# Kernel optimization log

Hardware: AMD Instinct MI355X
Metric: run time of the kernel (lower is better)

The kernel has to match this reference:

```python
import jax, jax.numpy as jnp
import numpy as np

BLOCK = 128


def setup_inputs() -> dict:
    key = jax.random.key(0)
    k_x, k_w, k_s, k_b = jax.random.split(key, 4)
    B, S, IN, OUT = 2, 2048, 4096, 4096
    x = jax.random.normal(k_x, (B, S, IN), dtype=jnp.float32)
    # fp8-quantized weight values (simulate e4m3 rounding, keep fp32 storage)
    w = jax.random.normal(k_w, (OUT, IN), dtype=jnp.float32) * 0.02
    weight = w.astype(jnp.float8_e4m3fn).astype(jnp.float32)
    # per-128x128-block inverse scales
    weight_scale_inv = jax.random.uniform(
        k_s, (OUT // BLOCK, IN // BLOCK), dtype=jnp.float32, minval=0.5, maxval=1.5)
    bias = jax.random.normal(k_b, (OUT,), dtype=jnp.float32) * 0.01
    return {"x": x, "weight": weight, "weight_scale_inv": weight_scale_inv, "bias": bias}


def _dequant(weight, scale_inv):
    # weight: [O, I], scale_inv: [O/128, I/128] -> broadcast each scale over a 128x128 block
    O, I = weight.shape
    w = weight.reshape(O // BLOCK, BLOCK, I // BLOCK, BLOCK)
    w = w * scale_inv[:, None, :, None]
    return w.reshape(O, I)


def reference(x, weight, weight_scale_inv, bias):
    w_deq = _dequant(weight, weight_scale_inv)          # [O, I]
    out = jnp.einsum('bsi,oi->bso', x, w_deq)           # [B, S, O]
    return out + bias
```

## Files before the change

### kernel.cpp

```cpp
#include <hip/hip_runtime.h>
#include <hip/hip_bf16.h>
#include <stdint.h>

typedef __attribute__((ext_vector_type(4))) float f32x4;
typedef __attribute__((ext_vector_type(8))) short short8;

__device__ __forceinline__ ushort f2b(float f) {
    union { __hip_bfloat16 h; ushort u; } c;
    c.h = __float2bfloat16(f);
    return c.u;
}

__device__ __forceinline__ void gload_lds16(const void* g, void* lds) {
    __builtin_amdgcn_global_load_lds((const __attribute__((address_space(1))) void*)g,
                                     (__attribute__((address_space(3))) void*)lds,
                                     16, 0, 0);
}

#define BARRIER()  asm volatile("s_barrier" ::: "memory")
#define VMCNT0()   asm volatile("s_waitcnt vmcnt(0)" ::: "memory")

__global__ void conv_both_kernel(const float* __restrict__ x, ushort* __restrict__ xb, long n8x,
                                 const float* __restrict__ w, const float* __restrict__ sinv,
                                 ushort* __restrict__ wb, int K, int nbk, long n8w) {
    long i = (long)blockIdx.x * blockDim.x + threadIdx.x;
    if (blockIdx.y == 0) {
        if (i >= n8x) return;
        const float4* xv = (const float4*)x;
        float4 v0 = xv[i * 2], v1 = xv[i * 2 + 1];
        short8 r;
        r[0] = (short)f2b(v0.x); r[1] = (short)f2b(v0.y); r[2] = (short)f2b(v0.z); r[3] = (short)f2b(v0.w);
        r[4] = (short)f2b(v1.x); r[5] = (short)f2b(v1.y); r[6] = (short)f2b(v1.z); r[7] = (short)f2b(v1.w);
        *(short8*)&xb[i * 8] = r;
    } else {
        if (i >= n8w) return;
        long e = i * 8;
        int o, c;
        if (K == 4096) { o = (int)(e >> 12); c = (int)(e & 4095); }
        else { o = (int)(e / K); c = (int)(e - (long)o * K); }
        const float s = sinv[(o >> 7) * nbk + (c >> 7)];
        const float4* wv = (const float4*)(w + e);
        float4 v0 = wv[0], v1 = wv[1];
        short8 r;
        r[0] = (short)f2b(v0.x * s); r[1] = (short)f2b(v0.y * s); r[2] = (short)f2b(v0.z * s); r[3] = (short)f2b(v0.w * s);
        r[4] = (short)f2b(v1.x * s); r[5] = (short)f2b(v1.y * s); r[6] = (short)f2b(v1.z * s); r[7] = (short)f2b(v1.w * s);
        *(short8*)&wb[e] = r;
    }
}

__global__ __launch_bounds__(512, 2)
void gemm256_kernel(const ushort* __restrict__ A, const ushort* __restrict__ Bm,
                    const float* __restrict__ bias, float* __restrict__ C,
                    int M, int N, int K) {
    __shared__ alignas(16) short sm[2][32768];

    const int tid  = threadIdx.x;
    const int lane = tid & 63;
    const int wid  = tid >> 6;
    const int wr   = wid >> 2;
    const int wc   = wid & 3;
    const int nbn  = N >> 8;

    const int nwg = gridDim.x;
    const int swz = (blockIdx.x & 7) * (nwg >> 3) + (blockIdx.x >> 3);
    const int bm  = swz / nbn;
    const int bn  = swz % nbn;

    const short* gA = (const short*)A + (size_t)bm * 256 * K;
    const short* gB = (const short*)Bm + (size_t)bn * 256 * K;

    const int srow = wid * 8 + (lane >> 3);
    const int scol = ((lane & 7) ^ (lane >> 3)) << 3;

    auto STAGE_A = [&](int U, int kt, int buf) {
        const short* src = gA + (size_t)(U * 64 + srow) * K + kt * 64 + scol;
        gload_lds16(src, &sm[buf][U * 4096 + wid * 512]);
    };
    auto STAGE_B = [&](int U, int kt, int buf) {
        const short* src = gB + (size_t)(U * 64 + srow) * K + kt * 64 + scol;
        gload_lds16(src, &sm[buf][16384 + U * 4096 + wid * 512]);
    };

    auto LD_A = [&](const short* Ab, int mh, int kk, short8 (&a)[4]) {
#pragma unroll
        for (int m = 0; m < 4; ++m) {
            int row = wr * 128 + mh * 64 + m * 16 + (lane & 15);
            a[m] = *(const short8*)&Ab[row * 64 + ((kk * 32 + (lane >> 4) * 8) ^ ((lane & 7) << 3))];
        }
    };
    auto LD_B = [&](const short* Bb, int kk, short8 (&b)[4]) {
#pragma unroll
        for (int n = 0; n < 4; ++n) {
            int row = wc * 64 + n * 16 + (lane & 15);
            b[n] = *(const short8*)&Bb[row * 64 + ((kk * 32 + (lane >> 4) * 8) ^ ((lane & 7) << 3))];
        }
    };

    f32x4 acc[8][4] = {};

    auto MFMA_H = [&](int off, short8 (&af)[4], short8 (&bf)[4], int m0, int m1) {
#pragma unroll
        for (int m = m0; m < m1; ++m)
#pragma unroll
            for (int n = 0; n < 4; ++n)
                acc[off + m][n] = __builtin_amdgcn_mfma_f32_16x16x32_bf16(af[m], bf[n], acc[off + m][n], 0, 0, 0);
    };

    const int nkt = K >> 6;

    short8 aCur[4], bCur[4];

    auto KSTEP = [&](int t) {
        const int b  = t & 1;
        const int tb = b ^ 1;
        const short* Ab  = &sm[b][0];
        const short* Bb  = &sm[b][16384];
        const short* AbN = &sm[tb][0];
        const short* BbN = &sm[tb][16384];
        const int tn = (t + 1 < nkt) ? t + 1 : nkt - 1;

        short8 aB[4], aC[4], aD[4], bB[4];

        BARRIER();
        __builtin_amdgcn_s_setprio(1);
        MFMA_H(0, aCur, bCur, 0, 2);
        LD_A(Ab, 1, 0, aB);
        MFMA_H(0, aCur, bCur, 2, 4);
        __builtin_amdgcn_s_setprio(0);
        STAGE_B(0, tn, tb); STAGE_B(1, tn, tb);
        STAGE_A(0, tn, tb); STAGE_A(2, tn, tb);

        BARRIER();
        __builtin_amdgcn_s_setprio(1);
        MFMA_H(4, aB, bCur, 0, 2);
        LD_A(Ab, 0, 1, aC);
        LD_B(Bb, 1, bB);
        MFMA_H(4, aB, bCur, 2, 4);
        __builtin_amdgcn_s_setprio(0);
        STAGE_A(1, tn, tb); STAGE_A(3, tn, tb);
        STAGE_B(2, tn, tb); STAGE_B(3, tn, tb);

        BARRIER();
        __builtin_amdgcn_s_setprio(1);
        MFMA_H(0, aC, bB, 0, 2);
        LD_A(Ab, 1, 1, aD);
        MFMA_H(0, aC, bB, 2, 4);
        __builtin_amdgcn_s_setprio(0);
        VMCNT0();

        BARRIER();
        __builtin_amdgcn_s_setprio(1);
        MFMA_H(4, aD, bB, 0, 2);
        LD_A(AbN, 0, 0, aCur);
        LD_B(BbN, 0, bCur);
        MFMA_H(4, aD, bB, 2, 4);
        __builtin_amdgcn_s_setprio(0);
    };

    {
        STAGE_B(0, 0, 0); STAGE_B(1, 0, 0);
        STAGE_A(0, 0, 0); STAGE_A(2, 0, 0);
        STAGE_A(1, 0, 0); STAGE_A(3, 0, 0);
        STAGE_B(2, 0, 0); STAGE_B(3, 0, 0);
        VMCNT0();
        BARRIER();
        LD_A(&sm[0][0], 0, 0, aCur);
        LD_B(&sm[0][16384], 0, bCur);
    }

    for (int t = 0; t < nkt; t += 2) {
        KSTEP(t);
        KSTEP(t + 1);
    }

    const int r0 = bm * 256 + wr * 128 + (lane >> 4) * 4;
    const int c0 = bn * 256 + wc * 64 + (lane & 15);
#pragma unroll
    for (int n = 0; n < 4; ++n) {
        float bv = bias[c0 + n * 16];
#pragma unroll
        for (int m = 0; m < 8; ++m) {
#pragma unroll
            for (int r = 0; r < 4; ++r) {
                C[(size_t)(r0 + m * 16 + r) * N + (c0 + n * 16)] = acc[m][n][r] + bv;
            }
        }
    }
}

__global__ void fallback_gemm(const float* __restrict__ x, const float* __restrict__ w,
                              const float* __restrict__ sinv, const float* __restrict__ bias,
                              float* __restrict__ out, int M, int N, int K) {
    int n = blockIdx.x * 64 + (threadIdx.x & 63);
    int m = blockIdx.y * 4 + (threadIdx.x >> 6);
    if (m >= M || n >= N) return;
    const int nbk = K >> 7;
    float acc = 0.f;
    for (int k = 0; k < K; ++k)
        acc += x[(size_t)m * K + k] * w[(size_t)n * K + k] * sinv[(n >> 7) * nbk + (k >> 7)];
    out[(size_t)m * N + n] = acc + bias[n];
}

extern "C" void kernel_launch(void* const* d_in, const int* in_sizes, int n_in,
                              void* d_out, int out_size, void* d_ws, size_t ws_size,
                              hipStream_t stream) {
    const float* x    = (const float*)d_in[0];
    const float* w    = (const float*)d_in[1];
    const float* sinv = (const float*)d_in[2];
    const float* bias = (const float*)d_in[3];
    float* out        = (float*)d_out;

    const int O = in_sizes[3];
    const int K = in_sizes[1] / O;
    const int M = (int)((long)in_sizes[0] / K);
    const int N = O;

    const size_t need = ((size_t)M * K + (size_t)N * K) * sizeof(ushort);
    const int nwg = (M / 256) * (N / 256);
    const bool ok = ws_size >= need && (M % 256 == 0) && (N % 256 == 0) &&
                    (K % 128 == 0) && (nwg % 8 == 0) && ((long)M * K % 2048 == 0) &&
                    (K % 2048 == 0);
    if (ok) {
        ushort* xb = (ushort*)d_ws;
        ushort* wb = xb + (size_t)M * K;
        long n8x = (long)M * K / 8;
        long n8w = (long)N * K / 8;
        long n8m = (n8x > n8w) ? n8x : n8w;
        dim3 cg((unsigned)((n8m + 255) / 256), 2);
        conv_both_kernel<<<cg, 256, 0, stream>>>(x, xb, n8x, w, sinv, wb, K, K >> 7, n8w);
        gemm256_kernel<<<dim3(nwg), 512, 0, stream>>>(xb, wb, bias, out, M, N, K);
    } else {
        dim3 g(N / 64, (M + 3) / 4);
        fallback_gemm<<<g, 256, 0, stream>>>(x, w, sinv, bias, out, M, N, K);
    }
}
```

Before: 282.5 us.

## Split LDS tiles into k-halves and pipeline loads with partial vmcnt waits

Reorganizes the shared-memory layout so each 64-wide K tile is stored as two 32-wide halves with a new XOR swizzle. Global-to-LDS staging is issued per half-tile and per operand, prefetching up to two k-tiles ahead. Each phase waits with partial vmcnt counts instead of a full drain. The aim is to keep more loads in flight and hide global memory latency, at the cost of a more delicate buffer-reuse ordering that could race if the counts are wrong.

```diff
diff --git a/kernel.cpp b/kernel.cpp
--- a/kernel.cpp
+++ b/kernel.cpp
@@ -18,7 +18,8 @@
 }
 
 #define BARRIER()  asm volatile("s_barrier" ::: "memory")
-#define VMCNT0()   asm volatile("s_waitcnt vmcnt(0)" ::: "memory")
+#define VMCNT6()   asm volatile("s_waitcnt vmcnt(6)" ::: "memory")
+#define VMCNT8()   asm volatile("s_waitcnt vmcnt(8)" ::: "memory")
 
 __global__ void conv_both_kernel(const float* __restrict__ x, ushort* __restrict__ xb, long n8x,
                                  const float* __restrict__ w, const float* __restrict__ sinv,
@@ -69,30 +70,28 @@
     const short* gA = (const short*)A + (size_t)bm * 256 * K;
     const short* gB = (const short*)Bm + (size_t)bn * 256 * K;
 
-    const int srow = wid * 8 + (lane >> 3);
-    const int scol = ((lane & 7) ^ (lane >> 3)) << 3;
-
-    auto STAGE_A = [&](int U, int kt, int buf) {
-        const short* src = gA + (size_t)(U * 64 + srow) * K + kt * 64 + scol;
-        gload_lds16(src, &sm[buf][U * 4096 + wid * 512]);
-    };
-    auto STAGE_B = [&](int U, int kt, int buf) {
-        const short* src = gB + (size_t)(U * 64 + srow) * K + kt * 64 + scol;
-        gload_lds16(src, &sm[buf][16384 + U * 4096 + wid * 512]);
-    };
-
-    auto LD_A = [&](const short* Ab, int mh, int kk, short8 (&a)[4]) {
+    auto STAGE = [&](const short* gOp, int opOff, int kh, int kt, int buf) {
+#pragma unroll
+        for (int g = 0; g < 2; ++g) {
+            int R = wid * 32 + g * 16 + (lane >> 2);
+            int chunk = (lane & 3) ^ ((R >> 1) & 3);
+            const short* src = gOp + (size_t)R * K + kt * 64 + kh * 32 + chunk * 8;
+            gload_lds16(src, &sm[buf][opOff + kh * 8192 + wid * 1024 + g * 512]);
+        }
+    };
+
+    auto LD_A = [&](int buf, int kh, int mh, short8 (&a)[4]) {
 #pragma unroll
         for (int m = 0; m < 4; ++m) {
             int row = wr * 128 + mh * 64 + m * 16 + (lane & 15);
-            a[m] = *(const short8*)&Ab[row * 64 + ((kk * 32 + (lane >> 4) * 8) ^ ((lane & 7) << 3))];
-        }
-    };
-    auto LD_B = [&](const short* Bb, int kk, short8 (&b)[4]) {
+            a[m] = *(const short8*)&sm[buf][kh * 8192 + row * 32 + ((((lane >> 4) ^ ((row >> 1) & 3))) << 3)];
+        }
+    };
+    auto LD_B = [&](int buf, int kh, short8 (&b)[4]) {
 #pragma unroll
         for (int n = 0; n < 4; ++n) {
             int row = wc * 64 + n * 16 + (lane & 15);
-            b[n] = *(const short8*)&Bb[row * 64 + ((kk * 32 + (lane >> 4) * 8) ^ ((lane & 7) << 3))];
+            b[n] = *(const short8*)&sm[buf][16384 + kh * 8192 + row * 32 + ((((lane >> 4) ^ ((row >> 1) & 3))) << 3)];
         }
     };
 
@@ -112,60 +111,62 @@
 
     auto KSTEP = [&](int t) {
         const int b  = t & 1;
-        const int tb = b ^ 1;
-        const short* Ab  = &sm[b][0];
-        const short* Bb  = &sm[b][16384];
-        const short* AbN = &sm[tb][0];
-        const short* BbN = &sm[tb][16384];
-        const int tn = (t + 1 < nkt) ? t + 1 : nkt - 1;
+        const int nb = b ^ 1;
+        const int t1 = (t + 1 < nkt) ? t + 1 : nkt - 1;
+        const int t2 = (t + 2 < nkt) ? t + 2 : nkt - 1;
 
         short8 aB[4], aC[4], aD[4], bB[4];
 
         BARRIER();
         __builtin_amdgcn_s_setprio(1);
         MFMA_H(0, aCur, bCur, 0, 2);
-        LD_A(Ab, 1, 0, aB);
+        LD_A(b, 0, 1, aB);
         MFMA_H(0, aCur, bCur, 2, 4);
         __builtin_amdgcn_s_setprio(0);
-        STAGE_B(0, tn, tb); STAGE_B(1, tn, tb);
-        STAGE_A(0, tn, tb); STAGE_A(2, tn, tb);
+        STAGE(gA, 0, 1, t1, nb);
+        VMCNT6();
 
         BARRIER();
         __builtin_amdgcn_s_setprio(1);
         MFMA_H(4, aB, bCur, 0, 2);
-        LD_A(Ab, 0, 1, aC);
-        LD_B(Bb, 1, bB);
+        LD_A(b, 1, 0, aC);
+        LD_B(b, 1, bB);
         MFMA_H(4, aB, bCur, 2, 4);
         __builtin_amdgcn_s_setprio(0);
-        STAGE_A(1, tn, tb); STAGE_A(3, tn, tb);
-        STAGE_B(2, tn, tb); STAGE_B(3, tn, tb);
+        STAGE(gB, 16384, 1, t1, nb);
+        VMCNT6();
 
         BARRIER();
         __builtin_amdgcn_s_setprio(1);
         MFMA_H(0, aC, bB, 0, 2);
-        LD_A(Ab, 1, 1, aD);
+        LD_A(b, 1, 1, aD);
         MFMA_H(0, aC, bB, 2, 4);
         __builtin_amdgcn_s_setprio(0);
-        VMCNT0();
+        STAGE(gA, 0, 0, t2, b);
+        VMCNT6();
 
         BARRIER();
         __builtin_amdgcn_s_setprio(1);
         MFMA_H(4, aD, bB, 0, 2);
-        LD_A(AbN, 0, 0, aCur);
-        LD_B(BbN, 0, bCur);
+        LD_A(nb, 0, 0, aCur);
+        LD_B(nb, 0, bCur);
         MFMA_H(4, aD, bB, 2, 4);
         __builtin_amdgcn_s_setprio(0);
+        STAGE(gB, 16384, 0, t2, b);
+        VMCNT6();
     };
 
     {
-        STAGE_B(0, 0, 0); STAGE_B(1, 0, 0);
-        STAGE_A(0, 0, 0); STAGE_A(2, 0, 0);
-        STAGE_A(1, 0, 0); STAGE_A(3, 0, 0);
-        STAGE_B(2, 0, 0); STAGE_B(3, 0, 0);
-        VMCNT0();
-        BARRIER();
-        LD_A(&sm[0][0], 0, 0, aCur);
-        LD_B(&sm[0][16384], 0, bCur);
+        STAGE(gA, 0, 0, 0, 0);
+        STAGE(gB, 16384, 0, 0, 0);
+        STAGE(gA, 0, 1, 0, 0);
+        STAGE(gB, 16384, 1, 0, 0);
+        STAGE(gA, 0, 0, 1, 1);
+        STAGE(gB, 16384, 0, 1, 1);
+        VMCNT8();
+        BARRIER();
+        LD_A(0, 0, 0, aCur);
+        LD_B(0, 0, bCur);
     }
 
     for (int t = 0; t < nkt; t += 2) {
```

After: 284.2 us. No clear change (+0.6%).
